# Kernel optimization log

Measured on AMD Instinct MI355X. Metric: run time of the kernel, lower is better.

## Reference

```python
import jax, jax.numpy as jnp
import numpy as np

NEG_SLOPE_GAT = 0.2   # PyG GATConv default negative_slope
NEG_SLOPE = 0.01      # torch.nn.LeakyReLU default
NUM_AISLES = 20       # aisle_nrs drawn from [0,20); matches aisle_nrs.max()+1


def leaky(x, s):
    return jnp.where(x >= 0, x, s * x)


def gat_conv(x, src, dst, W, a_src, a_dst, b, n_nodes):
    """Single-head PyG GATConv (self-loops already appended to src/dst)."""
    h = x @ W                                        # [N, C]
    es = h @ a_src                                   # [N]
    ed = h @ a_dst                                   # [N]
    e = leaky(es[src] + ed[dst], NEG_SLOPE_GAT)      # [E] per-edge score
    m = jax.ops.segment_max(e, dst, num_segments=n_nodes)
    w = jnp.exp(e - m[dst])
    z = jax.ops.segment_sum(w, dst, num_segments=n_nodes)
    alpha = w / z[dst]                               # segment softmax over incoming edges
    out = jax.ops.segment_sum(h[src] * alpha[:, None], dst, num_segments=n_nodes)
    return out + b


def setup_inputs() -> dict:
    key = jax.random.key(0)
    ks = jax.random.split(key, 32)
    B, N, E = 16, 2048, 32768
    Fin, H, O, HA = 32, 128, 64, 256

    def glorot(k, shape):
        fan = shape[0] + shape[-1]
        return jax.random.uniform(k, shape, jnp.float32, -1.0, 1.0) * np.sqrt(6.0 / fan)

    inp = {
        "graph_nodes": jax.random.normal(ks[0], (B, N, Fin), jnp.float32),
        "aisle_nrs": jax.random.randint(ks[1], (B, N), 0, NUM_AISLES),
        "graph_edge_links": jax.random.randint(ks[2], (B, 2, E), 0, N),
        "mask": jax.random.randint(ks[3], (B, N), 0, 2),
        "picks_left": jax.random.randint(ks[4], (B,), 0, 100),
        # GAT layer 1: Fin -> H
        "W1": glorot(ks[5], (Fin, H)), "as1": glorot(ks[6], (H,)), "ad1": glorot(ks[7], (H,)), "b1": jnp.zeros((H,), jnp.float32),
        # GAT layer 2: H -> H
        "W2": glorot(ks[8], (H, H)), "as2": glorot(ks[9], (H,)), "ad2": glorot(ks[10], (H,)), "b2": jnp.zeros((H,), jnp.float32),
        # GAT layer 3: H -> O
        "W3": glorot(ks[11], (H, O)), "as3": glorot(ks[12], (O,)), "ad3": glorot(ks[13], (O,)), "b3": jnp.zeros((O,), jnp.float32),
        # post-embedding MLP head
        "lw1": glorot(ks[14], (2 * O, HA)), "lb1": jnp.zeros((HA,), jnp.float32),
        "lw2": glorot(ks[15], (HA, O)), "lb2": jnp.zeros((O,), jnp.float32),
        "lw3": glorot(ks[16], (O, 1)), "lb3": jnp.zeros((1,), jnp.float32),
    }
    return inp


def reference(graph_nodes, aisle_nrs, graph_edge_links, mask, picks_left,
              W1, as1, ad1, b1, W2, as2, ad2, b2, W3, as3, ad3, b3,
              lw1, lb1, lw2, lb2, lw3, lb3):
    B, N, Fin = graph_nodes.shape
    NT = B * N
    x = graph_nodes.reshape(NT, Fin)

    # batch the graphs: offset per-graph edge indices, append self-loops
    off = (jnp.arange(B) * N)[:, None]
    src = (graph_edge_links[:, 0, :] + off).reshape(-1)
    dst = (graph_edge_links[:, 1, :] + off).reshape(-1)
    loops = jnp.arange(NT)
    src = jnp.concatenate([src, loops])
    dst = jnp.concatenate([dst, loops])

    x = gat_conv(x, src, dst, W1, as1, ad1, b1, NT)
    x = gat_conv(x, src, dst, W2, as2, ad2, b2, NT)
    x = gat_conv(x, src, dst, W3, as3, ad3, b3, NT)

    # scatter-mean aisle embedding
    batch_idx = jnp.repeat(jnp.arange(B), N)
    aid = aisle_nrs.reshape(-1) + batch_idx * NUM_AISLES   # [NT]
    S = B * NUM_AISLES
    ssum = jax.ops.segment_sum(x, aid, num_segments=S)
    cnt = jax.ops.segment_sum(jnp.ones((NT,), x.dtype), aid, num_segments=S)
    emb = ssum / jnp.maximum(cnt, 1.0)[:, None]

    x = jnp.concatenate([x, emb[aid]], axis=1)             # [NT, 2*O]
    x = leaky(x @ lw1 + lb1, NEG_SLOPE)
    x = leaky(x @ lw2 + lb2, NEG_SLOPE)
    x = (x @ lw3 + lb3).reshape(B, N)

    logits = jnp.where(mask != 0, x, -jnp.inf)
    return jax.nn.softmax(logits, axis=1)
```

## Files before the change

kernel.cpp:

```cpp
#include <hip/hip_runtime.h>
#include <hip/hip_bf16.h>
#include <math.h>

#define BATCH 16
#define NNODE 2048
#define EPG   32768
#define NT    (BATCH * NNODE)
#define ET    (BATCH * EPG + NT)
#define NUM_AISLES 20
#define SEG   (BATCH * NUM_AISLES)
#define NEG_GAT 0.2f
#define NEG_MLP 0.01f
#define ACHUNK 8
#define CAP 64

typedef __attribute__((ext_vector_type(8))) short s16x8;
typedef __attribute__((ext_vector_type(4))) float f32x4;

__device__ __forceinline__ void split_bf16(float v, unsigned short& hi, unsigned short& lo) {
    unsigned int u = __float_as_uint(v);
    unsigned int r = u + 0x7FFFu + ((u >> 16) & 1u);
    hi = (unsigned short)(r >> 16);
    float fh = __uint_as_float(((unsigned int)hi) << 16);
    float rem = v - fh;
    unsigned int u2 = __float_as_uint(rem);
    unsigned int r2 = u2 + 0x7FFFu + ((u2 >> 16) & 1u);
    lo = (unsigned short)(r2 >> 16);
}

__global__ __launch_bounds__(256) void edge_scatter(const int* __restrict__ links,
                                                    int* __restrict__ cnt,
                                                    int* __restrict__ col_bkt) {
    int b = blockIdx.x;
    int s, d;
    if (b < 2048) {
        int xcd = b & 7, idx = b >> 3;
        int g = xcd * 2 + (idx >> 7);
        int chunk = idx & 127;
        int i = chunk * 256 + threadIdx.x;
        const int* pb = links + (size_t)g * 2 * EPG;
        s = pb[i] + (g << 11);
        d = pb[EPG + i] + (g << 11);
    } else {
        int b2 = b - 2048;
        int xcd = b2 & 7, idx = b2 >> 3;
        int g = xcd * 2 + (idx >> 3);
        int chunk = idx & 7;
        s = d = g * NNODE + chunk * 256 + threadIdx.x;
    }
    int pos = atomicAdd(&cnt[d], 1);
    if (pos < CAP) col_bkt[d * CAP + pos] = s;
}

template <int K, int KC, int NOUT, int COLS, bool LEAKY, bool ATTN, bool FINAL, bool CONCAT>
__global__ __launch_bounds__(256) void gemm_mfma(const float* __restrict__ A,
                                                 const float* __restrict__ W,
                                                 const float* __restrict__ bias,
                                                 float* __restrict__ out,
                                                 const float* __restrict__ a_src,
                                                 const float* __restrict__ a_dst,
                                                 float* __restrict__ es,
                                                 float* __restrict__ ed,
                                                 const float* __restrict__ emb,
                                                 const int* __restrict__ aisle,
                                                 const float* __restrict__ lw3,
                                                 const float* __restrict__ lb3,
                                                 const int* __restrict__ mask,
                                                 float* __restrict__ logits) {
    constexpr int C = COLS / 16;
    constexpr int LDW = KC + 8;

    __shared__ unsigned short Wh[COLS * LDW], Wl[COLS * LDW];

    const int tid = threadIdx.x;
    const int wave = tid >> 6, lane = tid & 63;
    const int quad = lane >> 4, l15 = lane & 15;
    const int row0 = blockIdx.x * 64;
    const int c0 = blockIdx.y * COLS;
    const int m = row0 + wave * 16 + l15;

    f32x4 acc[C];
#pragma unroll
    for (int c = 0; c < C; ++c)
#pragma unroll
        for (int v = 0; v < 4; ++v) acc[c][v] = 0.f;

    union SU { s16x8 v; unsigned short u[8]; };

    for (int kb = 0; kb < K; kb += KC) {
        for (int i = tid; i < KC * COLS; i += 256) {
            int k = i / COLS;
            int n = i - k * COLS;
            unsigned short h, l;
            split_bf16(W[(size_t)(kb + k) * NOUT + c0 + n], h, l);
            Wh[n * LDW + k] = h;
            Wl[n * LDW + k] = l;
        }
        __syncthreads();

        for (int kc = kb; kc < kb + KC; kc += 32) {
            const int off = kc + quad * 8;
            const float* srcp;
            if constexpr (CONCAT) {
                if (off < 64) {
                    srcp = A + (size_t)m * 64 + off;
                } else {
                    int g = m >> 11;
                    srcp = emb + ((size_t)(g * NUM_AISLES + aisle[m])) * 64 + (off - 64);
                }
            } else {
                srcp = A + (size_t)m * K + off;
            }
            float4 v0 = ((const float4*)srcp)[0];
            float4 v1 = ((const float4*)srcp)[1];
            float a8[8] = {v0.x, v0.y, v0.z, v0.w, v1.x, v1.y, v1.z, v1.w};
            SU ah, al;
#pragma unroll
            for (int j = 0; j < 8; ++j) split_bf16(a8[j], ah.u[j], al.u[j]);

#pragma unroll
            for (int c = 0; c < C; ++c) {
                int woff = (c * 16 + l15) * LDW + (kc - kb) + quad * 8;
                s16x8 wh = *(const s16x8*)&Wh[woff];
                s16x8 wl = *(const s16x8*)&Wl[woff];
                acc[c] = __builtin_amdgcn_mfma_f32_16x16x32_bf16(ah.v, wh, acc[c], 0, 0, 0);
                acc[c] = __builtin_amdgcn_mfma_f32_16x16x32_bf16(ah.v, wl, acc[c], 0, 0, 0);
                acc[c] = __builtin_amdgcn_mfma_f32_16x16x32_bf16(al.v, wh, acc[c], 0, 0, 0);
            }
        }
        if (kb + KC < K) __syncthreads();
    }
    if constexpr (FINAL) {
#pragma unroll
        for (int reg = 0; reg < 4; ++reg) {
            float p = 0.f;
#pragma unroll
            for (int c = 0; c < C; ++c) {
                int colx = c * 16 + l15;
                float v = acc[c][reg] + bias[colx];
                v = v >= 0.f ? v : NEG_MLP * v;
                p += v * lw3[colx];
            }
#pragma unroll
            for (int mk = 1; mk < 16; mk <<= 1) p += __shfl_xor(p, mk, 64);
            if (l15 == 0) {
                int row = row0 + wave * 16 + quad * 4 + reg;
                float lg = p + lb3[0];
                logits[row] = (mask[row] != 0) ? lg : -INFINITY;
            }
        }
    } else {
#pragma unroll
        for (int c = 0; c < C; ++c) {
            int colx = c0 + c * 16 + l15;
            float bv = bias ? bias[colx] : 0.f;
#pragma unroll
            for (int reg = 0; reg < 4; ++reg) {
                int row = row0 + wave * 16 + quad * 4 + reg;
                float v = acc[c][reg] + bv;
                if (LEAKY) v = v >= 0.f ? v : NEG_MLP * v;
                out[(size_t)row * NOUT + colx] = v;
            }
        }
        if constexpr (ATTN) {
#pragma unroll
            for (int reg = 0; reg < 4; ++reg) {
                float ps = 0.f, pd = 0.f;
#pragma unroll
                for (int c = 0; c < C; ++c) {
                    int colx = c * 16 + l15;
                    float v = acc[c][reg];
                    ps += v * a_src[colx];
                    pd += v * a_dst[colx];
                }
#pragma unroll
                for (int mk = 1; mk < 16; mk <<= 1) {
                    ps += __shfl_xor(ps, mk, 64);
                    pd += __shfl_xor(pd, mk, 64);
                }
                if (l15 == 0) {
                    int row = row0 + wave * 16 + quad * 4 + reg;
                    es[row] = ps;
                    ed[row] = pd;
                }
            }
        }
    }
}

template <int HD>
__global__ __launch_bounds__(256) void gat_aggregate(const float* __restrict__ h,
                                                     const float* __restrict__ es,
                                                     const float* __restrict__ ed,
                                                     const int* __restrict__ cnt,
                                                     const int* __restrict__ col_bkt,
                                                     const float* __restrict__ bias,
                                                     float* __restrict__ out) {
    int b = blockIdx.x;
    int xcd = b & 7, q = b >> 3;
    int graph = xcd * 2 + (q >> 9);
    int node = graph * NNODE + (q & 511) * 4 + (threadIdx.x >> 6);
    int lane = threadIdx.x & 63;
    int deg = cnt[node];
    deg = deg < CAP ? deg : CAP;
    float edv = ed[node];

    float e0 = -INFINITY;
    int c0v = 0;
    if (lane < deg) {
        c0v = col_bkt[node * CAP + lane];
        float e = es[c0v] + edv;
        e0 = e >= 0.f ? e : NEG_GAT * e;
    }
    float m = e0;
#pragma unroll
    for (int off = 32; off; off >>= 1) m = fmaxf(m, __shfl_xor(m, off, 64));
    float z = __expf(e0 - m);
#pragma unroll
    for (int off = 32; off; off >>= 1) z += __shfl_xor(z, off, 64);
    float w0 = __expf(e0 - m) / z;

    const int quad = lane >> 4, l15 = lane & 15;
    if (HD == 128) {
        float a0 = 0.f, a1 = 0.f, a2 = 0.f, a3 = 0.f;
        float a4 = 0.f, a5 = 0.f, a6 = 0.f, a7 = 0.f;
        for (int jj = 0; jj < deg; jj += 4) {
            int j2 = jj + quad;
            int s = __shfl(c0v, j2, 64);
            float w = __shfl(w0, j2, 64);
            const float* base = h + (size_t)s * 128 + l15 * 8;
            float4 v0 = *(const float4*)base;
            float4 v1 = *(const float4*)(base + 4);
            a0 += w * v0.x; a1 += w * v0.y; a2 += w * v0.z; a3 += w * v0.w;
            a4 += w * v1.x; a5 += w * v1.y; a6 += w * v1.z; a7 += w * v1.w;
        }
#pragma unroll
        for (int off = 16; off <= 32; off <<= 1) {
            a0 += __shfl_xor(a0, off, 64); a1 += __shfl_xor(a1, off, 64);
            a2 += __shfl_xor(a2, off, 64); a3 += __shfl_xor(a3, off, 64);
            a4 += __shfl_xor(a4, off, 64); a5 += __shfl_xor(a5, off, 64);
            a6 += __shfl_xor(a6, off, 64); a7 += __shfl_xor(a7, off, 64);
        }
        if (quad == 0) {
            const float* bb = bias + l15 * 8;
            float4 o0, o1;
            o0.x = a0 + bb[0]; o0.y = a1 + bb[1]; o0.z = a2 + bb[2]; o0.w = a3 + bb[3];
            o1.x = a4 + bb[4]; o1.y = a5 + bb[5]; o1.z = a6 + bb[6]; o1.w = a7 + bb[7];
            float* op = out + (size_t)node * 128 + l15 * 8;
            *(float4*)op = o0;
            *(float4*)(op + 4) = o1;
        }
    } else {
        float a0 = 0.f, a1 = 0.f, a2 = 0.f, a3 = 0.f;
        for (int jj = 0; jj < deg; jj += 4) {
            int j2 = jj + quad;
            int s = __shfl(c0v, j2, 64);
            float w = __shfl(w0, j2, 64);
            float4 v = *(const float4*)(h + (size_t)s * 64 + l15 * 4);
            a0 += w * v.x; a1 += w * v.y; a2 += w * v.z; a3 += w * v.w;
        }
#pragma unroll
        for (int off = 16; off <= 32; off <<= 1) {
            a0 += __shfl_xor(a0, off, 64); a1 += __shfl_xor(a1, off, 64);
            a2 += __shfl_xor(a2, off, 64); a3 += __shfl_xor(a3, off, 64);
        }
        if (quad == 0) {
            const float* bb = bias + l15 * 4;
            float4 o;
            o.x = a0 + bb[0]; o.y = a1 + bb[1]; o.z = a2 + bb[2]; o.w = a3 + bb[3];
            *(float4*)(out + (size_t)node * 64 + l15 * 4) = o;
        }
    }
}

__global__ __launch_bounds__(256) void aisle_partial(const float* __restrict__ x3,
                                                     const int* __restrict__ aisle,
                                                     float* __restrict__ psum,
                                                     int* __restrict__ pcnt) {
    int g = blockIdx.x >> 3;
    int ch = blockIdx.x & 7;
    int f = threadIdx.x & 63;
    int stripe = threadIdx.x >> 6;

    __shared__ float sacc[4][NUM_AISLES][64];
    __shared__ int scnt[4][NUM_AISLES];
    for (int i = threadIdx.x; i < 4 * NUM_AISLES * 64; i += 256)
        ((float*)sacc)[i] = 0.f;
    for (int i = threadIdx.x; i < 4 * NUM_AISLES; i += 256)
        ((int*)scnt)[i] = 0;
    __syncthreads();

    const int* ai = aisle + g * NNODE;
    const float* xg = x3 + (size_t)g * NNODE * 64;
    int n0 = ch * 256 + stripe * 64;
#pragma unroll 4
    for (int i = 0; i < 64; ++i) {
        int n = n0 + i;
        int a = ai[n];
        float v = xg[(size_t)n * 64 + f];
        sacc[stripe][a][f] += v;
        if (f == 0) scnt[stripe][a]++;
    }
    __syncthreads();

    for (int i = threadIdx.x; i < NUM_AISLES * 64; i += 256) {
        int a = i >> 6, ff = i & 63;
        psum[((size_t)blockIdx.x * NUM_AISLES + a) * 64 + ff] =
            sacc[0][a][ff] + sacc[1][a][ff] + sacc[2][a][ff] + sacc[3][a][ff];
    }
    for (int i = threadIdx.x; i < NUM_AISLES; i += 256) {
        pcnt[blockIdx.x * NUM_AISLES + i] =
            scnt[0][i] + scnt[1][i] + scnt[2][i] + scnt[3][i];
    }
}

__global__ __launch_bounds__(256) void aisle_reduce(const float* __restrict__ psum,
                                                    const int* __restrict__ pcnt,
                                                    float* __restrict__ emb) {
    int idx = blockIdx.x * 256 + threadIdx.x;
    if (idx >= SEG * 64) return;
    int seg = idx >> 6;
    int f = idx & 63;
    int g = seg / NUM_AISLES;
    int a = seg - g * NUM_AISLES;
    float s = 0.f;
    int c = 0;
#pragma unroll
    for (int ch = 0; ch < ACHUNK; ++ch) {
        int blk = g * ACHUNK + ch;
        s += psum[((size_t)blk * NUM_AISLES + a) * 64 + f];
        c += pcnt[blk * NUM_AISLES + a];
    }
    emb[idx] = s / fmaxf((float)c, 1.0f);
}

__global__ __launch_bounds__(256) void softmax_kernel(const float* __restrict__ logits,
                                                      float* __restrict__ out) {
    int b = blockIdx.x;
    const float* lr = logits + b * NNODE;
    __shared__ float red[4], redz[4];
    float m = -INFINITY;
    for (int i = threadIdx.x; i < NNODE; i += 256) m = fmaxf(m, lr[i]);
#pragma unroll
    for (int off = 32; off; off >>= 1) m = fmaxf(m, __shfl_xor(m, off, 64));
    if ((threadIdx.x & 63) == 0) red[threadIdx.x >> 6] = m;
    __syncthreads();
    m = fmaxf(fmaxf(red[0], red[1]), fmaxf(red[2], red[3]));
    float z = 0.f;
    for (int i = threadIdx.x; i < NNODE; i += 256) z += __expf(lr[i] - m);
#pragma unroll
    for (int off = 32; off; off >>= 1) z += __shfl_xor(z, off, 64);
    if ((threadIdx.x & 63) == 0) redz[threadIdx.x >> 6] = z;
    __syncthreads();
    z = redz[0] + redz[1] + redz[2] + redz[3];
    float invz = 1.0f / z;
    for (int i = threadIdx.x; i < NNODE; i += 256) {
        float v = lr[i];
        out[b * NNODE + i] = (v == -INFINITY) ? 0.f : __expf(v - m) * invz;
    }
}


extern "C" void kernel_launch(void* const* d_in, const int* in_sizes, int n_in,
                              void* d_out, int out_size, void* d_ws, size_t ws_size,
                              hipStream_t stream) {
    const float* gn   = (const float*)d_in[0];
    const int* aisle  = (const int*)d_in[1];
    const int* links  = (const int*)d_in[2];
    const int* mask   = (const int*)d_in[3];
    const float* W1  = (const float*)d_in[5];
    const float* as1 = (const float*)d_in[6];
    const float* ad1 = (const float*)d_in[7];
    const float* b1  = (const float*)d_in[8];
    const float* W2  = (const float*)d_in[9];
    const float* as2 = (const float*)d_in[10];
    const float* ad2 = (const float*)d_in[11];
    const float* b2  = (const float*)d_in[12];
    const float* W3  = (const float*)d_in[13];
    const float* as3 = (const float*)d_in[14];
    const float* ad3 = (const float*)d_in[15];
    const float* b3  = (const float*)d_in[16];
    const float* lw1 = (const float*)d_in[17];
    const float* lb1 = (const float*)d_in[18];
    const float* lw2 = (const float*)d_in[19];
    const float* lb2 = (const float*)d_in[20];
    const float* lw3 = (const float*)d_in[21];
    const float* lb3 = (const float*)d_in[22];
    float* out = (float*)d_out;

    float* ws = (float*)d_ws;
    float* h      = ws;
    float* xb     = h + (size_t)NT * 128;
    float* es     = xb + (size_t)NT * 128;
    float* ed     = es + NT;
    float* emb    = ed + NT;
    float* y1     = emb + SEG * 64;
    float* y2     = y1 + (size_t)NT * 256;
    float* logits = y2 + (size_t)NT * 64;
    float* psum   = logits + NT;
    int* pcnt     = (int*)(psum + 128 * NUM_AISLES * 64);
    int* row_ptr  = pcnt + 128 * NUM_AISLES;
    int* cnt      = row_ptr + NT + 1;
    int* col_bkt  = (int*)y2;

    const int EB = (ET + 255) / 256;

    hipMemsetAsync(cnt, 0, NT * sizeof(int), stream);
    edge_scatter<<<EB, 256, 0, stream>>>(links, cnt, col_bkt);

    gemm_mfma<32, 32, 128, 128, false, true, false, false><<<dim3(NT / 64, 1), 256, 0, stream>>>(
        gn, W1, nullptr, h, as1, ad1, es, ed, nullptr, nullptr, nullptr, nullptr, nullptr, nullptr);
    gat_aggregate<128><<<NT / 4, 256, 0, stream>>>(h, es, ed, cnt, col_bkt, b1, xb);

    gemm_mfma<128, 64, 128, 128, false, true, false, false><<<dim3(NT / 64, 1), 256, 0, stream>>>(
        xb, W2, nullptr, h, as2, ad2, es, ed, nullptr, nullptr, nullptr, nullptr, nullptr, nullptr);
    gat_aggregate<128><<<NT / 4, 256, 0, stream>>>(h, es, ed, cnt, col_bkt, b2, xb);

    gemm_mfma<128, 128, 64, 64, false, true, false, false><<<dim3(NT / 64, 1), 256, 0, stream>>>(
        xb, W3, nullptr, h, as3, ad3, es, ed, nullptr, nullptr, nullptr, nullptr, nullptr, nullptr);
    gat_aggregate<64><<<NT / 4, 256, 0, stream>>>(h, es, ed, cnt, col_bkt, b3, xb);

    aisle_partial<<<BATCH * ACHUNK, 256, 0, stream>>>(xb, aisle, psum, pcnt);
    aisle_reduce<<<(SEG * 64 + 255) / 256, 256, 0, stream>>>(psum, pcnt, emb);

    gemm_mfma<128, 64, 256, 128, true, false, false, true><<<dim3(NT / 64, 2), 256, 0, stream>>>(
        xb, lw1, lb1, y1, nullptr, nullptr, nullptr, nullptr, emb, aisle, nullptr, nullptr, nullptr, nullptr);
    gemm_mfma<256, 128, 64, 64, true, false, true, false><<<dim3(NT / 64, 1), 256, 0, stream>>>(
        y1, lw2, lb2, y2, nullptr, nullptr, nullptr, nullptr, nullptr, nullptr, lw3, lb3, mask, logits);

    softmax_kernel<<<BATCH, 256, 0, stream>>>(logits, out);
}
```

Measured before the change: 306.9 us.

## Pre-split weights into swizzled bf16 tiles once and DMA them into LDS

Adds a prep kernel that splits every weight matrix into hi/lo bf16 once per call and stores each K-chunk tile in a pre-swizzled layout. The GEMM kernels then load tiles straight into LDS with global_load_lds instead of having each of 512 blocks re-split the fp32 weights. This removes redundant per-block conversion and strided global reads. It costs one extra kernel launch and some workspace, and moves from padded to XOR-swizzled LDS addressing.

```diff
diff --git a/kernel.cpp b/kernel.cpp
--- a/kernel.cpp
+++ b/kernel.cpp
@@ -1,6 +1,7 @@
 #include <hip/hip_runtime.h>
 #include <hip/hip_bf16.h>
 #include <math.h>
+#include <stdint.h>
 
 #define BATCH 16
 #define NNODE 2048
@@ -26,6 +27,40 @@
     unsigned int u2 = __float_as_uint(rem);
     unsigned int r2 = u2 + 0x7FFFu + ((u2 >> 16) & 1u);
     lo = (unsigned short)(r2 >> 16);
+}
+
+template <int K, int KC, int NOUT, int COLS>
+__device__ __forceinline__ void prep_one(const float* __restrict__ W,
+                                         unsigned short* __restrict__ dst, int idx) {
+    constexpr int SWM = (KC >= 64) ? 7 : 3;
+    int k = idx / NOUT, col = idx - k * NOUT;
+    int ch = k / KC, kl = k - ch * KC;
+    int ct = col / COLS, n = col - ct * COLS;
+    int tile = ct * (K / KC) + ch;
+    unsigned short h, l;
+    split_bf16(W[idx], h, l);
+    size_t base = (size_t)tile * (2 * COLS * KC);
+    int pos = n * KC + (kl ^ ((n & SWM) << 3));
+    dst[base + pos] = h;
+    dst[base + COLS * KC + pos] = l;
+}
+
+__global__ __launch_bounds__(256) void prep_weights(const float* __restrict__ W1,
+                                                    const float* __restrict__ W2,
+                                                    const float* __restrict__ W3,
+                                                    const float* __restrict__ lw1,
+                                                    const float* __restrict__ lw2,
+                                                    unsigned short* __restrict__ P1,
+                                                    unsigned short* __restrict__ P2,
+                                                    unsigned short* __restrict__ P3,
+                                                    unsigned short* __restrict__ P4,
+                                                    unsigned short* __restrict__ P5) {
+    int b = blockIdx.x, t = threadIdx.x;
+    if (b < 16)        prep_one<32, 32, 128, 128>(W1, P1, b * 256 + t);
+    else if (b < 80)   prep_one<128, 64, 128, 128>(W2, P2, (b - 16) * 256 + t);
+    else if (b < 112)  prep_one<128, 128, 64, 64>(W3, P3, (b - 80) * 256 + t);
+    else if (b < 240)  prep_one<128, 64, 256, 128>(lw1, P4, (b - 112) * 256 + t);
+    else               prep_one<256, 128, 64, 64>(lw2, P5, (b - 240) * 256 + t);
 }
 
 __global__ __launch_bounds__(256) void edge_scatter(const int* __restrict__ links,
@@ -54,7 +89,7 @@
 
 template <int K, int KC, int NOUT, int COLS, bool LEAKY, bool ATTN, bool FINAL, bool CONCAT>
 __global__ __launch_bounds__(256) void gemm_mfma(const float* __restrict__ A,
-                                                 const float* __restrict__ W,
+                                                 const unsigned short* __restrict__ WP,
                                                  const float* __restrict__ bias,
                                                  float* __restrict__ out,
                                                  const float* __restrict__ a_src,
@@ -68,15 +103,17 @@
                                                  const int* __restrict__ mask,
                                                  float* __restrict__ logits) {
     constexpr int C = COLS / 16;
-    constexpr int LDW = KC + 8;
-
-    __shared__ unsigned short Wh[COLS * LDW], Wl[COLS * LDW];
+    constexpr int SWM = (KC >= 64) ? 7 : 3;
+    constexpr int TILE_US = COLS * KC;
+    constexpr int TB2 = 2 * TILE_US * 2;
+    static_assert(TB2 % 4096 == 0, "chunk must be a multiple of one 256-thread 16B sweep");
+
+    __shared__ unsigned short WS[2 * TILE_US];
 
     const int tid = threadIdx.x;
     const int wave = tid >> 6, lane = tid & 63;
     const int quad = lane >> 4, l15 = lane & 15;
     const int row0 = blockIdx.x * 64;
-    const int c0 = blockIdx.y * COLS;
     const int m = row0 + wave * 16 + l15;
 
     f32x4 acc[C];
@@ -88,13 +125,14 @@
     union SU { s16x8 v; unsigned short u[8]; };
 
     for (int kb = 0; kb < K; kb += KC) {
-        for (int i = tid; i < KC * COLS; i += 256) {
-            int k = i / COLS;
-            int n = i - k * COLS;
-            unsigned short h, l;
-            split_bf16(W[(size_t)(kb + k) * NOUT + c0 + n], h, l);
-            Wh[n * LDW + k] = h;
-            Wl[n * LDW + k] = l;
+        const char* gsrc = (const char*)WP
+            + (size_t)(blockIdx.y * (K / KC) + kb / KC) * TB2;
+#pragma unroll
+        for (int s = 0; s < TB2 / 4096; ++s) {
+            __builtin_amdgcn_global_load_lds(
+                (const __attribute__((address_space(1))) void*)(gsrc + s * 4096 + wave * 1024 + lane * 16),
+                (__attribute__((address_space(3))) void*)&WS[(s * 4096 + wave * 1024) >> 1],
+                16, 0, 0);
         }
         __syncthreads();
 
@@ -118,11 +156,13 @@
 #pragma unroll
             for (int j = 0; j < 8; ++j) split_bf16(a8[j], ah.u[j], al.u[j]);
 
+            const int kq = (kc - kb) + quad * 8;
 #pragma unroll
             for (int c = 0; c < C; ++c) {
-                int woff = (c * 16 + l15) * LDW + (kc - kb) + quad * 8;
-                s16x8 wh = *(const s16x8*)&Wh[woff];
-                s16x8 wl = *(const s16x8*)&Wl[woff];
+                int n = c * 16 + l15;
+                int pos = n * KC + (kq ^ ((n & SWM) << 3));
+                s16x8 wh = *(const s16x8*)&WS[pos];
+                s16x8 wl = *(const s16x8*)&WS[TILE_US + pos];
                 acc[c] = __builtin_amdgcn_mfma_f32_16x16x32_bf16(ah.v, wh, acc[c], 0, 0, 0);
                 acc[c] = __builtin_amdgcn_mfma_f32_16x16x32_bf16(ah.v, wl, acc[c], 0, 0, 0);
                 acc[c] = __builtin_amdgcn_mfma_f32_16x16x32_bf16(al.v, wh, acc[c], 0, 0, 0);
@@ -152,7 +192,7 @@
     } else {
 #pragma unroll
         for (int c = 0; c < C; ++c) {
-            int colx = c0 + c * 16 + l15;
+            int colx = blockIdx.y * COLS + c * 16 + l15;
             float bv = bias ? bias[colx] : 0.f;
 #pragma unroll
             for (int reg = 0; reg < 4; ++reg) {
@@ -403,30 +443,38 @@
     int* cnt      = row_ptr + NT + 1;
     int* col_bkt  = (int*)y2;
 
+    unsigned short* wsplit = (unsigned short*)(((uintptr_t)(cnt + NT) + 255) & ~(uintptr_t)255);
+    unsigned short* P1 = wsplit;
+    unsigned short* P2 = P1 + 8192;
+    unsigned short* P3 = P2 + 32768;
+    unsigned short* P4 = P3 + 16384;
+    unsigned short* P5 = P4 + 65536;
+
     const int EB = (ET + 255) / 256;
 
     hipMemsetAsync(cnt, 0, NT * sizeof(int), stream);
+    prep_weights<<<304, 256, 0, stream>>>(W1, W2, W3, lw1, lw2, P1, P2, P3, P4, P5);
     edge_scatter<<<EB, 256, 0, stream>>>(links, cnt, col_bkt);
 
     gemm_mfma<32, 32, 128, 128, false, true, false, false><<<dim3(NT / 64, 1), 256, 0, stream>>>(
-        gn, W1, nullptr, h, as1, ad1, es, ed, nullptr, nullptr, nullptr, nullptr, nullptr, nullptr);
+        gn, P1, nullptr, h, as1, ad1, es, ed, nullptr, nullptr, nullptr, nullptr, nullptr, nullptr);
     gat_aggregate<128><<<NT / 4, 256, 0, stream>>>(h, es, ed, cnt, col_bkt, b1, xb);
 
     gemm_mfma<128, 64, 128, 128, false, true, false, false><<<dim3(NT / 64, 1), 256, 0, stream>>>(
-        xb, W2, nullptr, h, as2, ad2, es, ed, nullptr, nullptr, nullptr, nullptr, nullptr, nullptr);
+        xb, P2, nullptr, h, as2, ad2, es, ed, nullptr, nullptr, nullptr, nullptr, nullptr, nullptr);
     gat_aggregate<128><<<NT / 4, 256, 0, stream>>>(h, es, ed, cnt, col_bkt, b2, xb);
 
     gemm_mfma<128, 128, 64, 64, false, true, false, false><<<dim3(NT / 64, 1), 256, 0, stream>>>(
-        xb, W3, nullptr, h, as3, ad3, es, ed, nullptr, nullptr, nullptr, nullptr, nullptr, nullptr);
+        xb, P3, nullptr, h, as3, ad3, es, ed, nullptr, nullptr, nullptr, nullptr, nullptr, nullptr);
     gat_aggregate<64><<<NT / 4, 256, 0, stream>>>(h, es, ed, cnt, col_bkt, b3, xb);
 
     aisle_partial<<<BATCH * ACHUNK, 256, 0, stream>>>(xb, aisle, psum, pcnt);
     aisle_reduce<<<(SEG * 64 + 255) / 256, 256, 0, stream>>>(psum, pcnt, emb);
 
     gemm_mfma<128, 64, 256, 128, true, false, false, true><<<dim3(NT / 64, 2), 256, 0, stream>>>(
-        xb, lw1, lb1, y1, nullptr, nullptr, nullptr, nullptr, emb, aisle, nullptr, nullptr, nullptr, nullptr);
+        xb, P4, lb1, y1, nullptr, nullptr, nullptr, nullptr, emb, aisle, nullptr, nullptr, nullptr, nullptr);
     gemm_mfma<256, 128, 64, 64, true, false, true, false><<<dim3(NT / 64, 1), 256, 0, stream>>>(
-        y1, lw2, lb2, y2, nullptr, nullptr, nullptr, nullptr, nullptr, nullptr, lw3, lb3, mask, logits);
+        y1, P5, lb2, y2, nullptr, nullptr, nullptr, nullptr, nullptr, nullptr, lw3, lb3, mask, logits);
 
     softmax_kernel<<<BATCH, 256, 0, stream>>>(logits, out);
 }
```

Result: faster. 284.8 us (-7.2%).
